# Optimization experiments

Hardware: AMD Instinct MI355X
Metric: run time of the kernel (lower is better)

## Reference

```python
import jax, jax.numpy as jnp
import numpy as np

DIM = 1024
HEADS = 8
HEAD_DIM = DIM // HEADS
TAU = HEAD_DIM ** 0.5
BS, SEQ = 1, 2048


def setup_inputs() -> dict:
    key = jax.random.key(0)
    kq, kk, kv, kb = jax.random.split(key, 4)
    q = jax.random.normal(kq, (BS, SEQ, DIM), jnp.float32)
    k = jax.random.normal(kk, (BS, SEQ, DIM), jnp.float32)
    v = jax.random.normal(kv, (BS, SEQ, DIM), jnp.float32)
    Wi_w = jnp.zeros((HEADS, 3 * DIM), jnp.float32)
    Wi_b = 0.1 * jax.random.normal(kb, (HEADS,), jnp.float32)
    Wf_w = jnp.zeros((HEADS, 3 * DIM), jnp.float32)
    Wf_b = jnp.linspace(3.0, 6.0, HEADS, dtype=jnp.float32)  # equidistant_bias_init(3, 6)
    gn_w = jnp.ones((DIM,), jnp.float32)
    gn_b = jnp.zeros((DIM,), jnp.float32)
    return {"q": q, "k": k, "v": v, "Wi_w": Wi_w, "Wi_b": Wi_b,
            "Wf_w": Wf_w, "Wf_b": Wf_b, "gn_w": gn_w, "gn_b": gn_b}


def reference(q, k, v, Wi_w, Wi_b, Wf_w, Wf_b, gn_w, gn_b):
    bs, seq, dim = q.shape
    gate_in = jnp.concatenate([q, k, v], axis=-1)                    # [b, s, 3d]
    itilde = jnp.einsum('bsd,hd->bhs', gate_in, Wi_w) + Wi_b[None, :, None]
    ftilde = jnp.einsum('bsd,hd->bhs', gate_in, Wf_w) + Wf_b[None, :, None]

    # Decay matrix: F_act[i,j] = sum_{t=j+1..i} logsigmoid(ftilde_t), lower-tri else -inf
    csum = jnp.cumsum(jax.nn.log_sigmoid(ftilde), axis=-1)           # [b, h, s]
    Fmat = csum[..., :, None] - csum[..., None, :]                   # [b, h, s, s]
    mask = jnp.tril(jnp.ones((seq, seq), dtype=bool))
    F_act = jnp.where(mask, Fmat, -jnp.inf)

    Dtilde = F_act + itilde[..., None, :]                            # add input gate along j
    max_d = jnp.max(Dtilde, axis=-1, keepdims=True)
    D = jnp.exp(Dtilde - max_d)                                      # stabilized decay weights

    qh = q.reshape(bs, seq, HEADS, HEAD_DIM).transpose(0, 2, 1, 3)
    kh = k.reshape(bs, seq, HEADS, HEAD_DIM).transpose(0, 2, 1, 3)
    vh = v.reshape(bs, seq, HEADS, HEAD_DIM).transpose(0, 2, 1, 3)

    Ctilde = jnp.einsum('bhid,bhjd->bhij', qh, kh) * D / TAU
    maxit = jnp.maximum(jnp.abs(jnp.sum(Ctilde, axis=-1, keepdims=True)), jnp.exp(-max_d))
    Htilde = jnp.einsum('bhij,bhjd->bhid', Ctilde, vh) / (maxit + 1e-6)

    # GroupNorm(HEADS groups) over dim, applied per token
    x = Htilde.transpose(0, 2, 1, 3).reshape(bs * seq, HEADS, HEAD_DIM)
    mean = jnp.mean(x, axis=-1, keepdims=True)
    var = jnp.var(x, axis=-1, keepdims=True)
    xn = (x - mean) / jnp.sqrt(var + 1e-5)
    out = xn.reshape(bs * seq, DIM) * gn_w + gn_b
    return out.reshape(bs, seq, DIM)
```

## Files before the change

### kernel.cpp

```cpp
#include <hip/hip_runtime.h>
#include <math.h>

#define SEQ 2048
#define NH 8
#define HD 128
#define DIMF 1024
#define LOG2E 1.4426950408889634f
#define INVTAU 0.08838834764831845f

typedef __attribute__((ext_vector_type(8))) short bf16x8;
typedef __attribute__((ext_vector_type(8))) unsigned short us8;
typedef __attribute__((ext_vector_type(4))) float f32x4;
typedef __attribute__((ext_vector_type(16))) float f32x16;

__device__ float g_itacc[NH*SEQ];
__device__ float g_ftacc[NH*SEQ];
__device__ float g_aL[NH*SEQ];
__device__ float g_cmL[NH*SEQ];
__device__ float g_en[NH*SEQ];
__device__ unsigned short g_Qb[NH*SEQ*HD];
__device__ unsigned short g_Kb[NH*SEQ*HD];
__device__ unsigned short g_Vb[NH*SEQ*HD];
__device__ unsigned short g_Vt[NH*HD*SEQ];
__device__ unsigned short g_Wb[16*3072];

__device__ __forceinline__ unsigned short f2bf(float x) {
  unsigned u = __float_as_uint(x);
  u += 0x7fffu + ((u >> 16) & 1u);
  return (unsigned short)(u >> 16);
}

__device__ __forceinline__ unsigned packbf(float lo, float hi) {
  return (unsigned)f2bf(lo) | ((unsigned)f2bf(hi) << 16);
}

__global__ __launch_bounds__(256) void convert_kernel(const float* __restrict__ q,
                                                      const float* __restrict__ k,
                                                      const float* __restrict__ v,
                                                      const float* __restrict__ Wi,
                                                      const float* __restrict__ Wf) {
  const int bid = blockIdx.x;
  if (bid < 6144) {
    const int s = bid & 2047;
    const int t = bid >> 11;
    const float* src = (t == 0) ? q : (t == 1) ? k : v;
    unsigned short* dst = (t == 0) ? g_Qb : (t == 1) ? g_Kb : g_Vb;
    const int c = threadIdx.x * 4;
    const float4 f = *(const float4*)(src + s*DIMF + c);
    const int h = c >> 7, d = c & 127;
    ushort4 u;
    u.x = f2bf(f.x); u.y = f2bf(f.y); u.z = f2bf(f.z); u.w = f2bf(f.w);
    *(ushort4*)(dst + (h*SEQ + s)*HD + d) = u;
  } else {
    const int gid = (bid - 6144) * 256 + threadIdx.x;
    const int e4 = gid * 4;
    const int p = e4 / 3072;
    const int c = e4 % 3072;
    const float* src = (p < 8) ? (Wi + p*3072 + c) : (Wf + (p-8)*3072 + c);
    const float4 f = *(const float4*)src;
    ushort4 u;
    u.x = f2bf(f.x); u.y = f2bf(f.y); u.z = f2bf(f.z); u.w = f2bf(f.w);
    *(ushort4*)(g_Wb + p*3072 + c) = u;
  }
}

__global__ __launch_bounds__(256) void vtrans_kernel() {
  __shared__ __align__(16) unsigned short Ts[64*72];
  const int h  = blockIdx.x;
  const int s0 = blockIdx.y * 64;
  const int d0 = blockIdx.z * 64;
  const int t = threadIdx.x;
  {
    const int sr = t >> 2;
    const int c  = (t & 3) * 16;
    const unsigned short* src = g_Vb + (h*SEQ + s0 + sr)*HD + d0 + c;
    *(us8*)&Ts[sr*72 + c]     = *(const us8*)&src[0];
    *(us8*)&Ts[sr*72 + c + 8] = *(const us8*)&src[8];
  }
  __syncthreads();
  {
    const int w = t >> 6, l = t & 63;
    unsigned short outv[16];
    #pragma unroll
    for (int j = 0; j < 16; ++j) outv[j] = Ts[(w*16 + j)*72 + l];
    unsigned short* dst = g_Vt + (h*HD + d0 + l)*SEQ + s0 + w*16;
    *(us8*)&dst[0] = *(us8*)&outv[0];
    *(us8*)&dst[8] = *(us8*)&outv[8];
  }
}

__global__ __launch_bounds__(256) void gates_kernel() {
  __shared__ f32x4 red[4][64];
  const int tid = threadIdx.x;
  const int wave = tid >> 6, lane = tid & 63;
  const int q4 = lane >> 4, l16 = lane & 15;
  const int s0 = blockIdx.x * 16;
  f32x4 acc = {0.f, 0.f, 0.f, 0.f};
  #pragma unroll 8
  for (int ks = wave*24; ks < wave*24 + 24; ++ks) {
    const int k0 = ks*32 + q4*8;
    const int tsel = k0 >> 10;
    const int rem = k0 & 1023;
    const int hh = rem >> 7, dd = rem & 127;
    const unsigned short* base = (tsel == 0) ? g_Qb : (tsel == 1) ? g_Kb : g_Vb;
    const bf16x8 a = *(const bf16x8*)&base[(hh*SEQ + s0 + l16)*HD + dd];
    const bf16x8 b = *(const bf16x8*)&g_Wb[l16*3072 + k0];
    acc = __builtin_amdgcn_mfma_f32_16x16x32_bf16(a, b, acc, 0, 0, 0);
  }
  red[wave][lane] = acc;
  __syncthreads();
  if (wave == 0) {
    f32x4 s = red[0][lane];
    #pragma unroll
    for (int w = 1; w < 4; ++w) s += red[w][lane];
    #pragma unroll
    for (int r = 0; r < 4; ++r) {
      const int sg = s0 + 4*q4 + r;
      if (l16 < 8) g_itacc[l16*SEQ + sg] = s[r];
      else         g_ftacc[(l16-8)*SEQ + sg] = s[r];
    }
  }
}

__global__ __launch_bounds__(256) void scan_kernel(const float* __restrict__ Wi_b,
                                                   const float* __restrict__ Wf_b) {
  __shared__ float Wsum[4];
  __shared__ float Wmax[4];
  const int h = blockIdx.x;
  const int t = threadIdx.x;
  const int wave = t >> 6, lane = t & 63;
  const float ib = Wi_b[h];
  const float fb = Wf_b[h];
  const int base = h*SEQ + t*8;

  float it[8], ft[8];
  *(float4*)&it[0] = *(const float4*)&g_itacc[base];
  *(float4*)&it[4] = *(const float4*)&g_itacc[base+4];
  *(float4*)&ft[0] = *(const float4*)&g_ftacc[base];
  *(float4*)&ft[4] = *(const float4*)&g_ftacc[base+4];

  float cs[8];
  float run = 0.f;
  #pragma unroll
  for (int j = 0; j < 8; ++j) {
    const float f = ft[j] + fb;
    const float ls = fminf(f, 0.f) - log1pf(expf(-fabsf(f)));
    run += ls;
    cs[j] = run;
  }
  float x = run;
  #pragma unroll
  for (int off = 1; off < 64; off <<= 1) {
    const float tv = __shfl_up(x, off, 64);
    if (lane >= off) x += tv;
  }
  const float wexcl = x - run;
  if (lane == 63) Wsum[wave] = x;
  __syncthreads();
  float boff = 0.f;
  #pragma unroll
  for (int w = 0; w < 4; ++w) if (w < wave) boff += Wsum[w];
  const float cbase = boff + wexcl;

  float a[8], am[8], csum[8];
  float m = -__builtin_inff();
  #pragma unroll
  for (int j = 0; j < 8; ++j) {
    csum[j] = cbase + cs[j];
    a[j] = (it[j] + ib) - csum[j];
    m = fmaxf(m, a[j]);
    am[j] = m;
  }
  float y = m;
  #pragma unroll
  for (int off = 1; off < 64; off <<= 1) {
    const float tv = __shfl_up(y, off, 64);
    if (lane >= off) y = fmaxf(y, tv);
  }
  float e = __shfl_up(y, 1, 64);
  if (lane == 0) e = -__builtin_inff();
  if (lane == 63) Wmax[wave] = y;
  __syncthreads();
  float bmax = -__builtin_inff();
  #pragma unroll
  for (int w = 0; w < 4; ++w) if (w < wave) bmax = fmaxf(bmax, Wmax[w]);
  const float pre = fmaxf(bmax, e);

  float oa[8], ocm[8], oen[8];
  #pragma unroll
  for (int j = 0; j < 8; ++j) {
    const float cm = fmaxf(pre, am[j]);
    oa[j]  = a[j] * LOG2E;
    ocm[j] = cm * LOG2E;
    oen[j] = expf(-(csum[j] + cm));
  }
  *(float4*)&g_aL[base]    = *(float4*)&oa[0];
  *(float4*)&g_aL[base+4]  = *(float4*)&oa[4];
  *(float4*)&g_cmL[base]   = *(float4*)&ocm[0];
  *(float4*)&g_cmL[base+4] = *(float4*)&ocm[4];
  *(float4*)&g_en[base]    = *(float4*)&oen[0];
  *(float4*)&g_en[base+4]  = *(float4*)&oen[4];
}

__global__ __launch_bounds__(256, 2) void attn_kernel(const float* __restrict__ gnw,
                                                      const float* __restrict__ gnb,
                                                      float* __restrict__ out) {
  __shared__ __align__(16) us8 Ps[2][4][2][64];
  __shared__ float Sq[4][32];
  __shared__ float Sc[32];
  __shared__ float Sn1[4][32];
  __shared__ float Sn2[4][32];
  __shared__ float Mu[32];
  __shared__ float Rstd[32];

  const int h = blockIdx.x;
  const int y = blockIdx.y;
  const int t = (y < 32) ? (63 - y) : (y - 32);
  const int i0 = 32*t;
  const int imax = i0 + 31;
  const int nv = (imax >> 7) + 1;

  const int tid  = threadIdx.x;
  const int w    = tid >> 6;
  const int lane = tid & 63;
  const int l31  = lane & 31;
  const int hi   = lane >> 5;

  const unsigned short* Kgh = g_Kb + (h*SEQ + l31)*HD + hi*8;
  const unsigned short* Vgh = g_Vt + (h*HD + 32*w + l31)*SEQ + hi*8;
  const float*          aLh = g_aL + h*SEQ + 4*hi;

  bf16x8 qf[8];
  {
    const unsigned short* Qg = g_Qb + (h*SEQ + i0 + l31)*HD + hi*8;
    #pragma unroll
    for (int ks = 0; ks < 8; ++ks) qf[ks] = *(const bf16x8*)&Qg[ks*16];
  }
  const float cm = g_cmL[h*SEQ + i0 + l31];
  const int   ig = i0 + l31;

  f32x16 acc;
  #pragma unroll
  for (int e = 0; e < 16; ++e) acc[e] = 0.f;
  float rs = 0.f;

  for (int jc = 0; jc < nv; ++jc) {
    const int jb  = jc*128;
    const int jw  = jb + 32*w;
    const int buf = jc & 1;

    bf16x8 vb[8];
    #pragma unroll
    for (int q = 0; q < 4; ++q)
      #pragma unroll
      for (int ph = 0; ph < 2; ++ph)
        vb[q*2 + ph] = *(const bf16x8*)&Vgh[jb + q*32 + 16*ph];

    if (jw <= imax) {
      bf16x8 kf[8];
      #pragma unroll
      for (int ks = 0; ks < 8; ++ks) kf[ks] = *(const bf16x8*)&Kgh[jw*HD + ks*16];
      float4 aLq[4];
      #pragma unroll
      for (int rq = 0; rq < 4; ++rq) aLq[rq] = *(const float4*)&aLh[jw + 8*rq];

      f32x16 s;
      #pragma unroll
      for (int e = 0; e < 16; ++e) s[e] = 0.f;
      #pragma unroll
      for (int ks = 0; ks < 8; ++ks)
        s = __builtin_amdgcn_mfma_f32_32x32x16_bf16(kf[ks], qf[ks], s, 0, 0, 0);

      const bool needMask = (jw + 31 > i0);
      #pragma unroll
      for (int ph = 0; ph < 2; ++ph) {
        float pv[8];
        #pragma unroll
        for (int rr = 0; rr < 8; ++rr) {
          const int r  = 8*ph + rr;
          const int rq = r >> 2;
          const float aL = ((const float*)&aLq[rq])[r & 3];
          float p = s[r] * (exp2f(aL - cm) * INVTAU);
          if (needMask) {
            const int jg = jw + 8*rq + 4*hi + (r & 3);
            if (jg > ig) p = 0.f;
          }
          rs += p;
          pv[rr] = p;
        }
        const unsigned w0 = packbf(pv[0], pv[1]);
        const unsigned w1 = packbf(pv[2], pv[3]);
        const unsigned w2 = packbf(pv[4], pv[5]);
        const unsigned w3 = packbf(pv[6], pv[7]);
        const auto p0 = __builtin_amdgcn_permlane32_swap(w0, w2, false, false);
        const auto p1 = __builtin_amdgcn_permlane32_swap(w1, w3, false, false);
        union { unsigned u[4]; us8 sv; } fr;
        fr.u[0] = p0[0]; fr.u[1] = p1[0]; fr.u[2] = p0[1]; fr.u[3] = p1[1];
        Ps[buf][w][ph][lane] = fr.sv;
      }
    } else {
      const us8 z = {0, 0, 0, 0, 0, 0, 0, 0};
      Ps[buf][w][0][lane] = z;
      Ps[buf][w][1][lane] = z;
    }
    __syncthreads();

    #pragma unroll
    for (int q = 0; q < 4; ++q)
      #pragma unroll
      for (int ph = 0; ph < 2; ++ph) {
        const bf16x8 pf = *(const bf16x8*)&Ps[buf][q][ph][lane];
        acc = __builtin_amdgcn_mfma_f32_32x32x16_bf16(pf, vb[q*2 + ph], acc, 0, 0, 0);
      }
  }

  {
    const float rs2 = rs + __shfl_xor(rs, 32, 64);
    if (hi == 0) Sq[w][l31] = rs2;
  }
  __syncthreads();
  if (w == 0 && lane < 32) {
    const float S  = Sq[0][lane] + Sq[1][lane] + Sq[2][lane] + Sq[3][lane];
    const float en = g_en[h*SEQ + i0 + lane];
    Sc[lane] = 1.f / (fmaxf(fabsf(S), en) + 1e-6f);
  }
  __syncthreads();

  float o[16];
  #pragma unroll
  for (int r = 0; r < 16; ++r) {
    const int irow = (r & 3) + 8*(r >> 2) + 4*hi;
    const float xv = acc[r] * Sc[irow];
    o[r] = xv;
    float a = xv, b = xv * xv;
    #pragma unroll
    for (int m = 1; m < 32; m <<= 1) { a += __shfl_xor(a, m, 32); b += __shfl_xor(b, m, 32); }
    if (l31 == 0) { Sn1[w][irow] = a; Sn2[w][irow] = b; }
  }
  __syncthreads();
  if (w == 0 && lane < 32) {
    const float s1 = Sn1[0][lane] + Sn1[1][lane] + Sn1[2][lane] + Sn1[3][lane];
    const float s2 = Sn2[0][lane] + Sn2[1][lane] + Sn2[2][lane] + Sn2[3][lane];
    const float mean = s1 * (1.f/128.f);
    const float var  = s2 * (1.f/128.f) - mean*mean;
    Mu[lane]   = mean;
    Rstd[lane] = rsqrtf(var + 1e-5f);
  }
  __syncthreads();

  const float gwv = gnw[h*HD + 32*w + l31];
  const float gbv = gnb[h*HD + 32*w + l31];
  #pragma unroll
  for (int r = 0; r < 16; ++r) {
    const int irow = (r & 3) + 8*(r >> 2) + 4*hi;
    out[(i0 + irow)*DIMF + h*HD + 32*w + l31] =
        (o[r] - Mu[irow]) * Rstd[irow] * gwv + gbv;
  }
}

extern "C" void kernel_launch(void* const* d_in, const int* in_sizes, int n_in,
                              void* d_out, int out_size, void* d_ws, size_t ws_size,
                              hipStream_t stream) {
  (void)in_sizes; (void)n_in; (void)out_size; (void)d_ws; (void)ws_size;
  const float* q    = (const float*)d_in[0];
  const float* k    = (const float*)d_in[1];
  const float* v    = (const float*)d_in[2];
  const float* Wi_w = (const float*)d_in[3];
  const float* Wi_b = (const float*)d_in[4];
  const float* Wf_w = (const float*)d_in[5];
  const float* Wf_b = (const float*)d_in[6];
  const float* gnw  = (const float*)d_in[7];
  const float* gnb  = (const float*)d_in[8];
  float* out = (float*)d_out;

  convert_kernel<<<dim3(6192), 256, 0, stream>>>(q, k, v, Wi_w, Wf_w);
  vtrans_kernel<<<dim3(NH, SEQ/64, HD/64), 256, 0, stream>>>();
  gates_kernel<<<dim3(128), 256, 0, stream>>>();
  scan_kernel<<<dim3(NH), 256, 0, stream>>>(Wi_b, Wf_b);
  attn_kernel<<<dim3(NH, 64), 256, 0, stream>>>(gnw, gnb, out);
}
```

Baseline: 158.3 us.

## Use 8 waves per block splitting key chunks and reduce partial outputs in LDS

The attention kernel moves from 4 to 8 waves per block. Each iteration now covers 256 keys, and the two halves of the waves accumulate P·V for separate 128-key halves. The two partial accumulators are then summed through a shared-memory buffer before normalization. This halves the serial loop trip count per block and gives more waves to hide latency. In exchange it adds an LDS reduction, a large 56KB shared allocation, idle waves on causal-edge blocks, and lower occupancy (1 block per CU bound).

Measured after the change: 173.9 us. 9.9% more time.

```diff
diff --git a/kernel.cpp b/kernel.cpp
--- a/kernel.cpp
+++ b/kernel.cpp
@@ -202,11 +202,13 @@
   *(float4*)&g_en[base+4]  = *(float4*)&oen[4];
 }
 
-__global__ __launch_bounds__(256, 2) void attn_kernel(const float* __restrict__ gnw,
+__global__ __launch_bounds__(512, 1) void attn_kernel(const float* __restrict__ gnw,
                                                       const float* __restrict__ gnb,
                                                       float* __restrict__ out) {
-  __shared__ __align__(16) us8 Ps[2][4][2][64];
-  __shared__ float Sq[4][32];
+  __shared__ __align__(16) unsigned char smem[57344];
+  us8 (*Ps)[8][2][64] = (us8 (*)[8][2][64])smem;
+  float (*Ocomb)[32][33] = (float (*)[32][33])smem;
+  __shared__ float Sq[8][32];
   __shared__ float Sc[32];
   __shared__ float Sn1[4][32];
   __shared__ float Sn2[4][32];
@@ -218,16 +220,18 @@
   const int t = (y < 32) ? (63 - y) : (y - 32);
   const int i0 = 32*t;
   const int imax = i0 + 31;
-  const int nv = (imax >> 7) + 1;
+  const int nv = (imax >> 8) + 1;
 
   const int tid  = threadIdx.x;
   const int w    = tid >> 6;
   const int lane = tid & 63;
   const int l31  = lane & 31;
   const int hi   = lane >> 5;
+  const int dq   = w & 3;
+  const int jh   = w >> 2;
 
   const unsigned short* Kgh = g_Kb + (h*SEQ + l31)*HD + hi*8;
-  const unsigned short* Vgh = g_Vt + (h*HD + 32*w + l31)*SEQ + hi*8;
+  const unsigned short* Vgh = g_Vt + (h*HD + 32*dq + l31)*SEQ + hi*8;
   const float*          aLh = g_aL + h*SEQ + 4*hi;
 
   bf16x8 qf[8];
@@ -245,16 +249,16 @@
   float rs = 0.f;
 
   for (int jc = 0; jc < nv; ++jc) {
-    const int jb  = jc*128;
+    const int jb  = jc*256;
     const int jw  = jb + 32*w;
     const int buf = jc & 1;
 
     bf16x8 vb[8];
     #pragma unroll
-    for (int q = 0; q < 4; ++q)
+    for (int q2 = 0; q2 < 4; ++q2)
       #pragma unroll
       for (int ph = 0; ph < 2; ++ph)
-        vb[q*2 + ph] = *(const bf16x8*)&Vgh[jb + q*32 + 16*ph];
+        vb[q2*2 + ph] = *(const bf16x8*)&Vgh[jb + jh*128 + q2*32 + 16*ph];
 
     if (jw <= imax) {
       bf16x8 kf[8];
@@ -306,11 +310,11 @@
     __syncthreads();
 
     #pragma unroll
-    for (int q = 0; q < 4; ++q)
+    for (int q2 = 0; q2 < 4; ++q2)
       #pragma unroll
       for (int ph = 0; ph < 2; ++ph) {
-        const bf16x8 pf = *(const bf16x8*)&Ps[buf][q][ph][lane];
-        acc = __builtin_amdgcn_mfma_f32_32x32x16_bf16(pf, vb[q*2 + ph], acc, 0, 0, 0);
+        const bf16x8 pf = *(const bf16x8*)&Ps[buf][4*jh + q2][ph][lane];
+        acc = __builtin_amdgcn_mfma_f32_32x32x16_bf16(pf, vb[q2*2 + ph], acc, 0, 0, 0);
       }
   }
 
@@ -319,23 +323,34 @@
     if (hi == 0) Sq[w][l31] = rs2;
   }
   __syncthreads();
+  if (w >= 4) {
+    #pragma unroll
+    for (int r = 0; r < 16; ++r) {
+      const int row = (r & 3) + 8*(r >> 2) + 4*hi;
+      Ocomb[w - 4][row][l31] = acc[r];
+    }
+  }
   if (w == 0 && lane < 32) {
-    const float S  = Sq[0][lane] + Sq[1][lane] + Sq[2][lane] + Sq[3][lane];
+    float S = 0.f;
+    #pragma unroll
+    for (int k = 0; k < 8; ++k) S += Sq[k][lane];
     const float en = g_en[h*SEQ + i0 + lane];
     Sc[lane] = 1.f / (fmaxf(fabsf(S), en) + 1e-6f);
   }
   __syncthreads();
 
   float o[16];
-  #pragma unroll
-  for (int r = 0; r < 16; ++r) {
-    const int irow = (r & 3) + 8*(r >> 2) + 4*hi;
-    const float xv = acc[r] * Sc[irow];
-    o[r] = xv;
-    float a = xv, b = xv * xv;
-    #pragma unroll
-    for (int m = 1; m < 32; m <<= 1) { a += __shfl_xor(a, m, 32); b += __shfl_xor(b, m, 32); }
-    if (l31 == 0) { Sn1[w][irow] = a; Sn2[w][irow] = b; }
+  if (w < 4) {
+    #pragma unroll
+    for (int r = 0; r < 16; ++r) {
+      const int irow = (r & 3) + 8*(r >> 2) + 4*hi;
+      const float xv = (acc[r] + Ocomb[w][irow][l31]) * Sc[irow];
+      o[r] = xv;
+      float a = xv, b = xv * xv;
+      #pragma unroll
+      for (int m = 1; m < 32; m <<= 1) { a += __shfl_xor(a, m, 32); b += __shfl_xor(b, m, 32); }
+      if (l31 == 0) { Sn1[w][irow] = a; Sn2[w][irow] = b; }
+    }
   }
   __syncthreads();
   if (w == 0 && lane < 32) {
@@ -348,13 +363,15 @@
   }
   __syncthreads();
 
-  const float gwv = gnw[h*HD + 32*w + l31];
-  const float gbv = gnb[h*HD + 32*w + l31];
-  #pragma unroll
-  for (int r = 0; r < 16; ++r) {
-    const int irow = (r & 3) + 8*(r >> 2) + 4*hi;
-    out[(i0 + irow)*DIMF + h*HD + 32*w + l31] =
-        (o[r] - Mu[irow]) * Rstd[irow] * gwv + gbv;
+  if (w < 4) {
+    const float gwv = gnw[h*HD + 32*dq + l31];
+    const float gbv = gnb[h*HD + 32*dq + l31];
+    #pragma unroll
+    for (int r = 0; r < 16; ++r) {
+      const int irow = (r & 3) + 8*(r >> 2) + 4*hi;
+      out[(i0 + irow)*DIMF + h*HD + 32*dq + l31] =
+          (o[r] - Mu[irow]) * Rstd[irow] * gwv + gbv;
+    }
   }
 }
 
@@ -377,5 +394,5 @@
   vtrans_kernel<<<dim3(NH, SEQ/64, HD/64), 256, 0, stream>>>();
   gates_kernel<<<dim3(128), 256, 0, stream>>>();
   scan_kernel<<<dim3(NH), 256, 0, stream>>>(Wi_b, Wf_b);
-  attn_kernel<<<dim3(NH, 64), 256, 0, stream>>>(gnw, gnb, out);
-}
+  attn_kernel<<<dim3(NH, 64), 512, 0, stream>>>(gnw, gnb, out);
+}
```
